# Kernel optimization log

Hardware: AMD Instinct MI355X
Metric: run time of the kernel (lower is better)

The kernel has to match this reference:

```python
import jax, jax.numpy as jnp
import numpy as np

B, S, H = 2, 2048, 2048
NH, NKV = 16, 4
HD = H // NH            # 128
GROUPS = NH // NKV      # 4
ROTARY_BASE = 10000.0
NEG = -1e9


def setup_inputs() -> dict:
    key = jax.random.key(0)
    ks = jax.random.split(key, 6)
    x = jax.random.normal(ks[0], (B, S, H), dtype=jnp.float32)
    # additive causal mask [B,1,S,S]
    causal = jnp.where(jnp.tril(jnp.ones((S, S), dtype=bool)), 0.0, NEG).astype(jnp.float32)
    attention_mask = jnp.broadcast_to(causal[None, None], (B, 1, S, S))
    position_ids = jnp.broadcast_to(jnp.arange(S, dtype=jnp.int32)[None], (B, S))
    sc = 0.02
    Wq = jax.random.normal(ks[1], (H, NH * HD), dtype=jnp.float32) * sc
    Wk = jax.random.normal(ks[2], (H, NKV * HD), dtype=jnp.float32) * sc
    Wv = jax.random.normal(ks[3], (H, NKV * HD), dtype=jnp.float32) * sc
    Wo = jax.random.normal(ks[4], (H, H), dtype=jnp.float32) * sc
    return {"x": x, "attention_mask": attention_mask, "position_ids": position_ids,
            "Wq": Wq, "Wk": Wk, "Wv": Wv, "Wo": Wo}


def _rotate_half(t):
    t1, t2 = t[..., : HD // 2], t[..., HD // 2:]
    return jnp.concatenate((-t2, t1), axis=-1)


def _rope_sin_cos(position_ids, dtype):
    inv_freq = 1.0 / (ROTARY_BASE ** (jnp.arange(0, HD, 2, dtype=jnp.float32) / HD))  # [HD/2]
    freqs = position_ids.astype(jnp.float32)[..., None] * inv_freq[None, None, :]      # [B,S,HD/2]
    emb = jnp.concatenate((freqs, freqs), axis=-1)                                     # [B,S,HD]
    return jnp.sin(emb).astype(dtype), jnp.cos(emb).astype(dtype)


def reference(x, attention_mask, position_ids, Wq, Wk, Wv, Wo):
    # QKV projections (no bias)
    q = (x @ Wq).reshape(B, S, NH, HD).transpose(0, 2, 1, 3)     # [B,NH,S,HD]
    k = (x @ Wk).reshape(B, S, NKV, HD).transpose(0, 2, 1, 3)    # [B,NKV,S,HD]
    v = (x @ Wv).reshape(B, S, NKV, HD).transpose(0, 2, 1, 3)
    sin, cos = _rope_sin_cos(position_ids, x.dtype)
    sin, cos = sin[:, None], cos[:, None]                         # unsqueeze head dim
    q = q * cos + _rotate_half(q) * sin
    k = k * cos + _rotate_half(k) * sin
    # GQA: repeat kv heads
    k = jnp.repeat(k, GROUPS, axis=1)                             # [B,NH,S,HD]
    v = jnp.repeat(v, GROUPS, axis=1)
    scores = jnp.einsum('bhqd,bhkd->bhqk', q, k) / jnp.sqrt(jnp.asarray(HD, x.dtype))
    scores = scores + attention_mask                              # additive causal mask
    attn = jax.nn.softmax(scores.astype(jnp.float32), axis=-1).astype(x.dtype)
    # dropout p=0.0 -> no-op
    out = jnp.einsum('bhqk,bhkd->bhqd', attn, v)                  # [B,NH,S,HD]
    out = out.transpose(0, 2, 1, 3).reshape(B, S, H)
    return out @ Wo
```

## Files before the change

kernel.cpp:

```cpp
#include <hip/hip_runtime.h>
#include <hip/hip_bf16.h>
#include <stdint.h>
#include <math.h>

#define B_ 2
#define S_ 2048
#define H_ 2048
#define NH_ 16
#define NKV_ 4
#define HD_ 128

typedef __bf16 bf16;
typedef __bf16 bf16x8 __attribute__((ext_vector_type(8)));
typedef __bf16 bf16x4 __attribute__((ext_vector_type(4)));
typedef float f32x4 __attribute__((ext_vector_type(4)));

__device__ __forceinline__ void async_copy16(const void* g, void* l) {
  __builtin_amdgcn_global_load_lds(
      (const __attribute__((address_space(1))) void*)(uintptr_t)g,
      (__attribute__((address_space(3))) void*)(uintptr_t)l,
      16, 0, 0);
}

__device__ __forceinline__ f32x4 mfma16(bf16x8 a, bf16x8 b, f32x4 c) {
  return __builtin_amdgcn_mfma_f32_16x16x32_bf16(a, b, c, 0, 0, 0);
}


__global__ void f32_to_bf16_k(const float* __restrict__ in, bf16* __restrict__ o, int n) {
  int i = (blockIdx.x * 256 + threadIdx.x) * 4;
  if (i >= n) return;
  float4 v = *(const float4*)(in + i);
  bf16x4 r;
  r[0] = (bf16)v.x; r[1] = (bf16)v.y; r[2] = (bf16)v.z; r[3] = (bf16)v.w;
  *(bf16x4*)(o + i) = r;
}

__global__ void transpose_to_bf16_k(const float* __restrict__ W, bf16* __restrict__ Wt,
                                    int K, int N) {
  __shared__ float tile[32][33];
  int n0 = blockIdx.x * 32, k0 = blockIdx.y * 32;
  int tx = threadIdx.x, ty = threadIdx.y;
#pragma unroll
  for (int j = 0; j < 32; j += 8)
    tile[ty + j][tx] = W[(size_t)(k0 + ty + j) * N + n0 + tx];
  __syncthreads();
#pragma unroll
  for (int j = 0; j < 32; j += 8)
    Wt[(size_t)(n0 + ty + j) * K + k0 + tx] = (bf16)tile[tx][ty + j];
}

__global__ void rope_table_k(float2* __restrict__ tab) {
  int i = blockIdx.x * 256 + threadIdx.x;
  int p = i >> 6, d = i & 63;
  float invf = expf(-((float)(2 * d) / 128.0f) * 9.210340371976184f);
  float fr = (float)p * invf;
  float sv, cv;
  sincosf(fr, &sv, &cv);
  tab[i] = make_float2(cv, sv);
}

__global__ void rope_apply_k(bf16* __restrict__ t, const int* __restrict__ pos_ids,
                             const float2* __restrict__ tab, int hshift, int hmask,
                             float scale) {
  int i = blockIdx.x * 256 + threadIdx.x;
  int d = i & 63;
  int tmp = i >> 6;
  int h = tmp & hmask;
  int row = tmp >> hshift;
  int pos = pos_ids[row];
  float2 cs = tab[pos * 64 + d];
  size_t base = (((size_t)row << hshift) + h) * HD_;
  float a = (float)t[base + d];
  float b = (float)t[base + d + 64];
  t[base + d]      = (bf16)((a * cs.x - b * cs.y) * scale);
  t[base + d + 64] = (bf16)((b * cs.x + a * cs.y) * scale);
}


template <bool OUT_F32>
__global__ __launch_bounds__(512) void gemm8_k(const bf16* __restrict__ A,
                                               const bf16* __restrict__ Bt,
                                               void* __restrict__ Cv,
                                               int M, int N, int K) {
  extern __shared__ __align__(16) char smem[];
  const int tid = threadIdx.x;
  const int lane = tid & 63;
  const int w = tid >> 6;
  const int wm = w >> 2;
  const int wn = w & 3;
  const int g16 = lane >> 4, c16 = lane & 15;
  const int row0 = blockIdx.y * 128;
  const int col0 = blockIdx.x * 256;
  const int srow = tid >> 3;
  const int sslot = tid & 7;
  const int ldsw = w * 1024;

  auto stageA = [&](int s, int kt, int r) {
    int row = r * 64 + srow;
    int ss = sslot ^ (row & 7);
    async_copy16(A + (size_t)(row0 + row) * K + (kt << 6) + ss * 8,
                 smem + s * 49152 + r * 8192 + ldsw);
  };
  auto stageB = [&](int s, int kt, int r) {
    int row = r * 64 + srow;
    int ss = sslot ^ (row & 7);
    async_copy16(Bt + (size_t)(col0 + row) * K + (kt << 6) + ss * 8,
                 smem + s * 49152 + 16384 + r * 8192 + ldsw);
  };

  int offA[2][4], offB[2][4];
#pragma unroll
  for (int ks = 0; ks < 2; ++ks) {
#pragma unroll
    for (int i = 0; i < 4; ++i) {
      int ra = wm * 64 + i * 16 + c16;
      offA[ks][i] = ra * 128 + (((ks * 4 + g16) ^ (ra & 7)) << 4);
      int rb = wn * 64 + i * 16 + c16;
      offB[ks][i] = rb * 128 + (((ks * 4 + g16) ^ (rb & 7)) << 4);
    }
  }

  const f32x4 fz = {0.f, 0.f, 0.f, 0.f};
  f32x4 acc[4][4];
#pragma unroll
  for (int i = 0; i < 4; ++i)
#pragma unroll
    for (int j = 0; j < 4; ++j) acc[i][j] = fz;

  const int nkt = K >> 6;
#pragma unroll
  for (int r = 0; r < 2; ++r) stageA(0, 0, r);
#pragma unroll
  for (int r = 0; r < 4; ++r) stageB(0, 0, r);
#pragma unroll
  for (int r = 0; r < 2; ++r) stageA(1, 1, r);
#pragma unroll
  for (int r = 0; r < 4; ++r) stageB(1, 1, r);
  asm volatile("s_waitcnt vmcnt(6)" ::: "memory");
  __builtin_amdgcn_s_barrier();

  int ct = 0, pt = 2;
  for (int t = 0; t < nkt; ++t) {
    const char* Ab = smem + ct * 49152;
    const char* Bb = Ab + 16384;
    const bool pf = (t + 2 < nkt);
    const int kpf = t + 2;
    bf16x8 a0[4], a1[4], bx[2];

#pragma unroll
    for (int i = 0; i < 4; ++i) a0[i] = *(const bf16x8*)(Ab + offA[0][i]);
    bx[0] = *(const bf16x8*)(Bb + offB[0][0]);
    bx[1] = *(const bf16x8*)(Bb + offB[0][1]);
    if (pf) { stageA(pt, kpf, 0); stageA(pt, kpf, 1); }
    asm volatile("" ::: "memory");
    __builtin_amdgcn_s_barrier();
    asm volatile("s_waitcnt lgkmcnt(0)" ::: "memory");
    __builtin_amdgcn_sched_barrier(0);
    __builtin_amdgcn_s_setprio(1);
#pragma unroll
    for (int i = 0; i < 4; ++i) {
      acc[i][0] = mfma16(a0[i], bx[0], acc[i][0]);
      acc[i][1] = mfma16(a0[i], bx[1], acc[i][1]);
    }
    __builtin_amdgcn_s_setprio(0);
    __builtin_amdgcn_sched_barrier(0);
    asm volatile("" ::: "memory");
    __builtin_amdgcn_s_barrier();

    bx[0] = *(const bf16x8*)(Bb + offB[0][2]);
    bx[1] = *(const bf16x8*)(Bb + offB[0][3]);
    if (pf) { stageB(pt, kpf, 0); stageB(pt, kpf, 1); }
    asm volatile("" ::: "memory");
    __builtin_amdgcn_s_barrier();
    asm volatile("s_waitcnt lgkmcnt(0)" ::: "memory");
    __builtin_amdgcn_sched_barrier(0);
    __builtin_amdgcn_s_setprio(1);
#pragma unroll
    for (int i = 0; i < 4; ++i) {
      acc[i][2] = mfma16(a0[i], bx[0], acc[i][2]);
      acc[i][3] = mfma16(a0[i], bx[1], acc[i][3]);
    }
    __builtin_amdgcn_s_setprio(0);
    __builtin_amdgcn_sched_barrier(0);
    asm volatile("" ::: "memory");
    __builtin_amdgcn_s_barrier();

#pragma unroll
    for (int i = 0; i < 4; ++i) a1[i] = *(const bf16x8*)(Ab + offA[1][i]);
    bx[0] = *(const bf16x8*)(Bb + offB[1][0]);
    bx[1] = *(const bf16x8*)(Bb + offB[1][1]);
    if (pf) { stageB(pt, kpf, 2); stageB(pt, kpf, 3); }
    asm volatile("" ::: "memory");
    __builtin_amdgcn_s_barrier();
    asm volatile("s_waitcnt lgkmcnt(0)" ::: "memory");
    __builtin_amdgcn_sched_barrier(0);
    __builtin_amdgcn_s_setprio(1);
#pragma unroll
    for (int i = 0; i < 4; ++i) {
      acc[i][0] = mfma16(a1[i], bx[0], acc[i][0]);
      acc[i][1] = mfma16(a1[i], bx[1], acc[i][1]);
    }
    __builtin_amdgcn_s_setprio(0);
    __builtin_amdgcn_sched_barrier(0);
    asm volatile("" ::: "memory");
    __builtin_amdgcn_s_barrier();

    bx[0] = *(const bf16x8*)(Bb + offB[1][2]);
    bx[1] = *(const bf16x8*)(Bb + offB[1][3]);
    if (pf) asm volatile("s_waitcnt vmcnt(6)" ::: "memory");
    else    asm volatile("s_waitcnt vmcnt(0)" ::: "memory");
    __builtin_amdgcn_s_barrier();
    asm volatile("s_waitcnt lgkmcnt(0)" ::: "memory");
    __builtin_amdgcn_sched_barrier(0);
    __builtin_amdgcn_s_setprio(1);
#pragma unroll
    for (int i = 0; i < 4; ++i) {
      acc[i][2] = mfma16(a1[i], bx[0], acc[i][2]);
      acc[i][3] = mfma16(a1[i], bx[1], acc[i][3]);
    }
    __builtin_amdgcn_s_setprio(0);
    __builtin_amdgcn_sched_barrier(0);
    asm volatile("" ::: "memory");
    __builtin_amdgcn_s_barrier();

    ct = (ct == 2) ? 0 : ct + 1;
    pt = (pt == 2) ? 0 : pt + 1;
  }

#pragma unroll
  for (int i = 0; i < 4; ++i) {
    int gr0 = row0 + wm * 64 + i * 16 + g16 * 4;
#pragma unroll
    for (int j = 0; j < 4; ++j) {
      int gc = col0 + wn * 64 + j * 16 + c16;
#pragma unroll
      for (int r = 0; r < 4; ++r) {
        if constexpr (OUT_F32)
          ((float*)Cv)[(size_t)(gr0 + r) * N + gc] = acc[i][j][r];
        else
          ((bf16*)Cv)[(size_t)(gr0 + r) * N + gc] = (bf16)acc[i][j][r];
      }
    }
  }
}


template <bool OUT_F32, bool VT_Z1>
__global__ __launch_bounds__(256) void gemm_bt_k(const bf16* __restrict__ A,
                                                 const bf16* __restrict__ Bt0,
                                                 const bf16* __restrict__ Bt1,
                                                 void* __restrict__ C0, void* __restrict__ C1,
                                                 int M, int N, int K) {
  const bf16* __restrict__ Bt = (blockIdx.z == 0) ? Bt0 : Bt1;
  void* C = (blockIdx.z == 0) ? C0 : C1;
  __shared__ __align__(16) bf16 As[128 * 64];
  __shared__ __align__(16) bf16 Bs[128 * 64];
  const int tid = threadIdx.x;
  const int lane = tid & 63;
  const int w = tid >> 6;
  const int wm = w >> 1, wn = w & 1;
  const int g16 = lane >> 4, c16 = lane & 15;
  const int row0 = blockIdx.y * 128;
  const int col0 = blockIdx.x * 128;
  const int sr = lane >> 3;
  const int st = lane & 7;
  const int ss = st ^ sr;

  const f32x4 fz = {0.f, 0.f, 0.f, 0.f};
  f32x4 acc[4][4];
#pragma unroll
  for (int i = 0; i < 4; ++i)
#pragma unroll
    for (int j = 0; j < 4; ++j) acc[i][j] = fz;

  const int nkt = K >> 6;
  for (int kt = 0; kt < nkt; ++kt) {
    const int k0 = kt << 6;
    __syncthreads();
#pragma unroll
    for (int c = 0; c < 4; ++c) {
      int rbase = w * 32 + c * 8;
      async_copy16(A + (size_t)(row0 + rbase + sr) * K + k0 + ss * 8,
                   (char*)As + rbase * 128);
      async_copy16(Bt + (size_t)(col0 + rbase + sr) * K + k0 + ss * 8,
                   (char*)Bs + rbase * 128);
    }
    __syncthreads();
#pragma unroll
    for (int ks = 0; ks < 2; ++ks) {
      bf16x8 af[4], bfr[4];
#pragma unroll
      for (int t = 0; t < 4; ++t) {
        int ra = wm * 64 + t * 16 + c16;
        af[t] = *(const bf16x8*)((const char*)As + ra * 128 + (((ks * 4 + g16) ^ (ra & 7)) << 4));
        int rb = wn * 64 + t * 16 + c16;
        bfr[t] = *(const bf16x8*)((const char*)Bs + rb * 128 + (((ks * 4 + g16) ^ (rb & 7)) << 4));
      }
#pragma unroll
      for (int i = 0; i < 4; ++i)
#pragma unroll
        for (int j = 0; j < 4; ++j) acc[i][j] = mfma16(af[i], bfr[j], acc[i][j]);
    }
  }

  const bool vt = VT_Z1 && (blockIdx.z == 1);
#pragma unroll
  for (int i = 0; i < 4; ++i) {
    int gr0 = row0 + wm * 64 + i * 16 + g16 * 4;
#pragma unroll
    for (int j = 0; j < 4; ++j) {
      int gc = col0 + wn * 64 + j * 16 + c16;
      if (vt) {
        size_t va = ((size_t)((gr0 >> 11) * NKV_ + (gc >> 7)) * HD_ + (gc & 127)) * S_ + (gr0 & 2047);
        bf16x4 pk;
#pragma unroll
        for (int r = 0; r < 4; ++r) pk[r] = (bf16)acc[i][j][r];
        *(bf16x4*)((bf16*)C + va) = pk;
      } else {
#pragma unroll
        for (int r = 0; r < 4; ++r) {
          if constexpr (OUT_F32)
            ((float*)C)[(size_t)(gr0 + r) * N + gc] = acc[i][j][r];
          else
            ((bf16*)C)[(size_t)(gr0 + r) * N + gc] = (bf16)acc[i][j][r];
        }
      }
    }
  }
}


__global__ __launch_bounds__(256, 2) void attn_fwd_k(const bf16* __restrict__ Qg,
                                                     const bf16* __restrict__ Kg,
                                                     const bf16* __restrict__ VTg,
                                                     bf16* __restrict__ Og) {
  __shared__ __align__(16) bf16 Ks[2][64 * 128];
  __shared__ __align__(16) bf16 Vt[2][128 * 64];

  const int tid = threadIdx.x;
  const int lane = tid & 63;
  const int w = tid >> 6;
  const int g16 = lane >> 4;
  const int c16 = lane & 15;

  int bid = blockIdx.x;
  int rr_ = bid >> 5, bh = bid & 31;
  int qb = (rr_ < 8) ? (15 - rr_) : (rr_ - 8);
  const int b = bh >> 4;
  const int h = bh & 15;
  const int hkv = h >> 2;
  const int q0 = qb * 128;
  const int qw = q0 + w * 32;

  bf16x8 qf[2][4];
#pragma unroll
  for (int nq = 0; nq < 2; ++nq)
#pragma unroll
    for (int ksq = 0; ksq < 4; ++ksq)
      qf[nq][ksq] = *(const bf16x8*)(Qg + ((size_t)(b * S_ + qw + nq * 16 + c16) * NH_ + h) * HD_ + (ksq * 4 + g16) * 8);

  float m_run[2] = {-1e30f, -1e30f};
  float l_run[2] = {0.f, 0.f};
  const f32x4 fz = {0.f, 0.f, 0.f, 0.f};
  f32x4 acc[2][8];
#pragma unroll
  for (int nq = 0; nq < 2; ++nq)
#pragma unroll
    for (int dt = 0; dt < 8; ++dt) acc[nq][dt] = fz;

  const size_t kbase = ((size_t)b * S_ * NKV_ + hkv) * HD_;
  const size_t vbase = ((size_t)(b * NKV_ + hkv)) * HD_ * S_;

  auto stage = [&](int buf, int kv0) {
#pragma unroll
    for (int rd = 0; rd < 4; ++rd) {
      int Lb = rd * 256 + w * 64;
      int row = (Lb + lane) >> 4;
      int ssl = (lane & 15) ^ (row & 7);
      async_copy16(Kg + kbase + (size_t)(kv0 + row) * (NKV_ * HD_) + ssl * 8,
                   (char*)&Ks[buf][0] + Lb * 16);
    }
#pragma unroll
    for (int rd = 0; rd < 4; ++rd) {
      int Lb = rd * 256 + w * 64;
      int row = (Lb + lane) >> 3;
      int ssl = (lane & 7) ^ (row & 7);
      async_copy16(VTg + vbase + (size_t)row * S_ + kv0 + ssl * 8,
                   (char*)&Vt[buf][0] + Lb * 16);
    }
  };

  const int ntiles = 2 * qb + 2;
  stage(0, 0);
  int cur = 0;

  for (int t = 0; t < ntiles; ++t) {
    __syncthreads();
    if (t + 1 < ntiles) stage(cur ^ 1, (t + 1) * 64);
    const int kv0 = t * 64;

    if (kv0 <= qw + 31) {
      const bf16* KsC = &Ks[cur][0];
      const bf16* VtC = &Vt[cur][0];

      f32x4 sc[2][4];
#pragma unroll
      for (int nq = 0; nq < 2; ++nq)
#pragma unroll
        for (int mt = 0; mt < 4; ++mt) sc[nq][mt] = fz;

#pragma unroll
      for (int ksq = 0; ksq < 4; ++ksq) {
        bf16x8 kf[4];
#pragma unroll
        for (int mt = 0; mt < 4; ++mt) {
          int gp = c16 >> 2, rp = c16 & 3;
          int blk = 8 * (mt >> 1) + 2 * gp + ((mt & 1) ^ (gp & 1));
          int row = blk * 4 + rp;
          kf[mt] = *(const bf16x8*)((const char*)KsC + row * 256 + (((ksq * 4 + g16) ^ (row & 7)) << 4));
        }
#pragma unroll
        for (int nq = 0; nq < 2; ++nq)
#pragma unroll
          for (int mt = 0; mt < 4; ++mt)
            sc[nq][mt] = mfma16(kf[mt], qf[nq][ksq], sc[nq][mt]);
      }

      if (kv0 + 63 > qw) {
#pragma unroll
        for (int nq = 0; nq < 2; ++nq) {
          int qa = qw + nq * 16 + c16;
#pragma unroll
          for (int mt = 0; mt < 4; ++mt) {
            int blk = 8 * (mt >> 1) + 2 * g16 + ((mt & 1) ^ (g16 & 1));
#pragma unroll
            for (int r = 0; r < 4; ++r) {
              int ka = kv0 + blk * 4 + r;
              if (ka > qa) sc[nq][mt][r] = -1e30f;
            }
          }
        }
      }

      float mx[2];
#pragma unroll
      for (int nq = 0; nq < 2; ++nq) {
        float v = sc[nq][0][0];
#pragma unroll
        for (int mt = 0; mt < 4; ++mt)
#pragma unroll
          for (int r = 0; r < 4; ++r) v = fmaxf(v, sc[nq][mt][r]);
        v = fmaxf(v, __shfl_xor(v, 16));
        v = fmaxf(v, __shfl_xor(v, 32));
        mx[nq] = v;
      }
      if (__any((mx[0] > m_run[0] + 8.f) || (mx[1] > m_run[1] + 8.f))) {
#pragma unroll
        for (int nq = 0; nq < 2; ++nq) {
          float mn = fmaxf(m_run[nq], mx[nq]);
          float corr = exp2f(m_run[nq] - mn);
          m_run[nq] = mn;
          l_run[nq] *= corr;
#pragma unroll
          for (int dt = 0; dt < 8; ++dt) acc[nq][dt] *= corr;
        }
      }
#pragma unroll
      for (int nq = 0; nq < 2; ++nq) {
        float sum = 0.f;
#pragma unroll
        for (int mt = 0; mt < 4; ++mt)
#pragma unroll
          for (int r = 0; r < 4; ++r) {
            float p = exp2f(sc[nq][mt][r] - m_run[nq]);
            sc[nq][mt][r] = p;
            sum += p;
          }
        sum += __shfl_xor(sum, 16);
        sum += __shfl_xor(sum, 32);
        l_run[nq] += sum;
      }

      bf16x8 pa[2][2];
#pragma unroll
      for (int nq = 0; nq < 2; ++nq)
#pragma unroll
        for (int ks = 0; ks < 2; ++ks) {
          f32x4 sA = (g16 & 1) ? sc[nq][2 * ks + 1] : sc[nq][2 * ks];
          f32x4 sB = (g16 & 1) ? sc[nq][2 * ks] : sc[nq][2 * ks + 1];
          bf16x8 tf;
          tf[0] = (bf16)sA[0]; tf[1] = (bf16)sA[1]; tf[2] = (bf16)sA[2]; tf[3] = (bf16)sA[3];
          tf[4] = (bf16)sB[0]; tf[5] = (bf16)sB[1]; tf[6] = (bf16)sB[2]; tf[7] = (bf16)sB[3];
          pa[nq][ks] = tf;
        }

#pragma unroll
      for (int ks = 0; ks < 2; ++ks)
#pragma unroll
        for (int dt = 0; dt < 8; ++dt) {
          int rv = dt * 16 + c16;
          bf16x8 vf = *(const bf16x8*)((const char*)VtC + rv * 128 + (((ks * 4 + g16) ^ (rv & 7)) << 4));
          acc[0][dt] = mfma16(vf, pa[0][ks], acc[0][dt]);
          acc[1][dt] = mfma16(vf, pa[1][ks], acc[1][dt]);
        }
    }
    cur ^= 1;
  }

#pragma unroll
  for (int nq = 0; nq < 2; ++nq) {
    float inv = 1.0f / l_run[nq];
    size_t base = ((size_t)(b * S_ + qw + nq * 16 + c16) * NH_ + h) * HD_ + g16 * 4;
#pragma unroll
    for (int dt = 0; dt < 8; ++dt) {
      bf16x4 ov;
#pragma unroll
      for (int r = 0; r < 4; ++r) ov[r] = (bf16)(acc[nq][dt][r] * inv);
      *(bf16x4*)(Og + base + dt * 16) = ov;
    }
  }
}


extern "C" void kernel_launch(void* const* d_in, const int* in_sizes, int n_in,
                              void* d_out, int out_size, void* d_ws, size_t ws_size,
                              hipStream_t stream) {
  const float* x  = (const float*)d_in[0];
  const int* pos  = (const int*)d_in[2];
  const float* Wq = (const float*)d_in[3];
  const float* Wk = (const float*)d_in[4];
  const float* Wv = (const float*)d_in[5];
  const float* Wo = (const float*)d_in[6];

  char* ws = (char*)d_ws;
  size_t off = 0;
  auto alloc = [&](size_t bytes) -> char* {
    char* p = ws + off;
    off += (bytes + 255) & ~(size_t)255;
    return p;
  };
  const size_t rows = (size_t)B_ * S_;
  bf16* xb   = (bf16*)alloc(rows * H_ * 2);
  bf16* bq   = (bf16*)alloc(rows * (NH_ * HD_) * 2);
  bf16* batt = (bf16*)alloc(rows * (NH_ * HD_) * 2);
  bf16* WqT  = (bf16*)alloc((size_t)H_ * (NH_ * HD_) * 2);
  bf16* WoT  = (bf16*)alloc((size_t)H_ * H_ * 2);
  bf16* bk   = (bf16*)alloc(rows * (NKV_ * HD_) * 2);
  bf16* VT   = (bf16*)alloc(rows * (NKV_ * HD_) * 2);
  bf16* WkT  = (bf16*)alloc((size_t)H_ * (NKV_ * HD_) * 2);
  bf16* WvT  = (bf16*)alloc((size_t)H_ * (NKV_ * HD_) * 2);
  float2* tab = (float2*)alloc((size_t)S_ * 64 * sizeof(float2));

  auto* fq = gemm8_k<false>;
  auto* fo = gemm8_k<true>;
  const int dynlds = 3 * 49152;
  bool big =
      (hipFuncSetAttribute((const void*)fq, hipFuncAttributeMaxDynamicSharedMemorySize, dynlds) == hipSuccess) &&
      (hipFuncSetAttribute((const void*)fo, hipFuncAttributeMaxDynamicSharedMemorySize, dynlds) == hipSuccess);

  f32_to_bf16_k<<<(rows * H_) / (256 * 4), 256, 0, stream>>>(x, xb, rows * H_);
  transpose_to_bf16_k<<<dim3(H_ / 32, H_ / 32), dim3(32, 8), 0, stream>>>(Wq, WqT, H_, NH_ * HD_);
  transpose_to_bf16_k<<<dim3((NKV_ * HD_) / 32, H_ / 32), dim3(32, 8), 0, stream>>>(Wk, WkT, H_, NKV_ * HD_);
  transpose_to_bf16_k<<<dim3((NKV_ * HD_) / 32, H_ / 32), dim3(32, 8), 0, stream>>>(Wv, WvT, H_, NKV_ * HD_);
  transpose_to_bf16_k<<<dim3(H_ / 32, H_ / 32), dim3(32, 8), 0, stream>>>(Wo, WoT, H_, H_);
  rope_table_k<<<(S_ * 64) / 256, 256, 0, stream>>>(tab);

  if (big)
    gemm8_k<false><<<dim3(8, 32), 512, dynlds, stream>>>(xb, WqT, bq, 4096, 2048, 2048);
  else
    gemm_bt_k<false, false><<<dim3(16, 32, 1), 256, 0, stream>>>(xb, WqT, WqT, bq, bq, 4096, 2048, 2048);

  gemm_bt_k<false, true><<<dim3(4, 32, 2), 256, 0, stream>>>(xb, WkT, WvT, bk, VT, 4096, 512, 2048);

  rope_apply_k<<<(4096 * NH_ * 64) / 256, 256, 0, stream>>>(bq, pos, tab, 4, 15, 0.12753102f);
  rope_apply_k<<<(4096 * NKV_ * 64) / 256, 256, 0, stream>>>(bk, pos, tab, 2, 3, 1.0f);

  attn_fwd_k<<<dim3(512), 256, 0, stream>>>(bq, bk, VT, batt);

  if (big)
    gemm8_k<true><<<dim3(8, 32), 512, dynlds, stream>>>(batt, WoT, d_out, 4096, 2048, 2048);
  else
    gemm_bt_k<true, false><<<dim3(16, 32, 1), 256, 0, stream>>>(batt, WoT, WoT, d_out, d_out, 4096, 2048, 2048);
}
```

Before: 226.9 us.

## Fuse QKV projections into one GEMM, widen attention warps, simplify GEMM pipeline

```diff
diff --git a/kernel.cpp b/kernel.cpp
--- a/kernel.cpp
+++ b/kernel.cpp
@@ -78,10 +78,12 @@
 }
 
 
-template <bool OUT_F32>
+template <int MODE>
 __global__ __launch_bounds__(512) void gemm8_k(const bf16* __restrict__ A,
                                                const bf16* __restrict__ Bt,
-                                               void* __restrict__ Cv,
+                                               void* __restrict__ C0,
+                                               void* __restrict__ C1,
+                                               void* __restrict__ C2,
                                                int M, int N, int K) {
   extern __shared__ __align__(16) char smem[];
   const int tid = threadIdx.x;
@@ -146,68 +148,30 @@
     const char* Bb = Ab + 16384;
     const bool pf = (t + 2 < nkt);
     const int kpf = t + 2;
-    bf16x8 a0[4], a1[4], bx[2];
-
-#pragma unroll
-    for (int i = 0; i < 4; ++i) a0[i] = *(const bf16x8*)(Ab + offA[0][i]);
-    bx[0] = *(const bf16x8*)(Bb + offB[0][0]);
-    bx[1] = *(const bf16x8*)(Bb + offB[0][1]);
-    if (pf) { stageA(pt, kpf, 0); stageA(pt, kpf, 1); }
-    asm volatile("" ::: "memory");
+    bf16x8 af[4], bfr[4];
+
+#pragma unroll
+    for (int i = 0; i < 4; ++i) af[i] = *(const bf16x8*)(Ab + offA[0][i]);
+#pragma unroll
+    for (int j = 0; j < 4; ++j) bfr[j] = *(const bf16x8*)(Bb + offB[0][j]);
+    if (pf) { stageA(pt, kpf, 0); stageA(pt, kpf, 1); stageB(pt, kpf, 0); }
     __builtin_amdgcn_s_barrier();
     asm volatile("s_waitcnt lgkmcnt(0)" ::: "memory");
     __builtin_amdgcn_sched_barrier(0);
     __builtin_amdgcn_s_setprio(1);
 #pragma unroll
-    for (int i = 0; i < 4; ++i) {
-      acc[i][0] = mfma16(a0[i], bx[0], acc[i][0]);
-      acc[i][1] = mfma16(a0[i], bx[1], acc[i][1]);
-    }
+    for (int i = 0; i < 4; ++i)
+#pragma unroll
+      for (int j = 0; j < 4; ++j) acc[i][j] = mfma16(af[i], bfr[j], acc[i][j]);
     __builtin_amdgcn_s_setprio(0);
     __builtin_amdgcn_sched_barrier(0);
-    asm volatile("" ::: "memory");
     __builtin_amdgcn_s_barrier();
 
-    bx[0] = *(const bf16x8*)(Bb + offB[0][2]);
-    bx[1] = *(const bf16x8*)(Bb + offB[0][3]);
-    if (pf) { stageB(pt, kpf, 0); stageB(pt, kpf, 1); }
-    asm volatile("" ::: "memory");
-    __builtin_amdgcn_s_barrier();
-    asm volatile("s_waitcnt lgkmcnt(0)" ::: "memory");
-    __builtin_amdgcn_sched_barrier(0);
-    __builtin_amdgcn_s_setprio(1);
-#pragma unroll
-    for (int i = 0; i < 4; ++i) {
-      acc[i][2] = mfma16(a0[i], bx[0], acc[i][2]);
-      acc[i][3] = mfma16(a0[i], bx[1], acc[i][3]);
-    }
-    __builtin_amdgcn_s_setprio(0);
-    __builtin_amdgcn_sched_barrier(0);
-    asm volatile("" ::: "memory");
-    __builtin_amdgcn_s_barrier();
-
-#pragma unroll
-    for (int i = 0; i < 4; ++i) a1[i] = *(const bf16x8*)(Ab + offA[1][i]);
-    bx[0] = *(const bf16x8*)(Bb + offB[1][0]);
-    bx[1] = *(const bf16x8*)(Bb + offB[1][1]);
-    if (pf) { stageB(pt, kpf, 2); stageB(pt, kpf, 3); }
-    asm volatile("" ::: "memory");
-    __builtin_amdgcn_s_barrier();
-    asm volatile("s_waitcnt lgkmcnt(0)" ::: "memory");
-    __builtin_amdgcn_sched_barrier(0);
-    __builtin_amdgcn_s_setprio(1);
-#pragma unroll
-    for (int i = 0; i < 4; ++i) {
-      acc[i][0] = mfma16(a1[i], bx[0], acc[i][0]);
-      acc[i][1] = mfma16(a1[i], bx[1], acc[i][1]);
-    }
-    __builtin_amdgcn_s_setprio(0);
-    __builtin_amdgcn_sched_barrier(0);
-    asm volatile("" ::: "memory");
-    __builtin_amdgcn_s_barrier();
-
-    bx[0] = *(const bf16x8*)(Bb + offB[1][2]);
-    bx[1] = *(const bf16x8*)(Bb + offB[1][3]);
+#pragma unroll
+    for (int i = 0; i < 4; ++i) af[i] = *(const bf16x8*)(Ab + offA[1][i]);
+#pragma unroll
+    for (int j = 0; j < 4; ++j) bfr[j] = *(const bf16x8*)(Bb + offB[1][j]);
+    if (pf) { stageB(pt, kpf, 1); stageB(pt, kpf, 2); stageB(pt, kpf, 3); }
     if (pf) asm volatile("s_waitcnt vmcnt(6)" ::: "memory");
     else    asm volatile("s_waitcnt vmcnt(0)" ::: "memory");
     __builtin_amdgcn_s_barrier();
@@ -215,13 +179,11 @@
     __builtin_amdgcn_sched_barrier(0);
     __builtin_amdgcn_s_setprio(1);
 #pragma unroll
-    for (int i = 0; i < 4; ++i) {
-      acc[i][2] = mfma16(a1[i], bx[0], acc[i][2]);
-      acc[i][3] = mfma16(a1[i], bx[1], acc[i][3]);
-    }
+    for (int i = 0; i < 4; ++i)
+#pragma unroll
+      for (int j = 0; j < 4; ++j) acc[i][j] = mfma16(af[i], bfr[j], acc[i][j]);
     __builtin_amdgcn_s_setprio(0);
     __builtin_amdgcn_sched_barrier(0);
-    asm volatile("" ::: "memory");
     __builtin_amdgcn_s_barrier();
 
     ct = (ct == 2) ? 0 : ct + 1;
@@ -234,12 +196,32 @@
 #pragma unroll
     for (int j = 0; j < 4; ++j) {
       int gc = col0 + wn * 64 + j * 16 + c16;
-#pragma unroll
-      for (int r = 0; r < 4; ++r) {
-        if constexpr (OUT_F32)
-          ((float*)Cv)[(size_t)(gr0 + r) * N + gc] = acc[i][j][r];
-        else
-          ((bf16*)Cv)[(size_t)(gr0 + r) * N + gc] = (bf16)acc[i][j][r];
+      if constexpr (MODE == 2) {
+        if (col0 < 2048) {
+#pragma unroll
+          for (int r = 0; r < 4; ++r)
+            ((bf16*)C0)[(size_t)(gr0 + r) * 2048 + gc] = (bf16)acc[i][j][r];
+        } else if (col0 < 2560) {
+#pragma unroll
+          for (int r = 0; r < 4; ++r)
+            ((bf16*)C1)[(size_t)(gr0 + r) * 512 + (gc - 2048)] = (bf16)acc[i][j][r];
+        } else {
+          int dv = gc - 2560;
+          int hkv = dv >> 7, d = dv & 127;
+          size_t va = (((size_t)(gr0 >> 11) * NKV_ + hkv) * HD_ + d) * S_ + (gr0 & 2047);
+          bf16x4 pk;
+#pragma unroll
+          for (int r = 0; r < 4; ++r) pk[r] = (bf16)acc[i][j][r];
+          *(bf16x4*)((bf16*)C2 + va) = pk;
+        }
+      } else {
+#pragma unroll
+        for (int r = 0; r < 4; ++r) {
+          if constexpr (MODE == 1)
+            ((float*)C0)[(size_t)(gr0 + r) * N + gc] = acc[i][j][r];
+          else
+            ((bf16*)C0)[(size_t)(gr0 + r) * N + gc] = (bf16)acc[i][j][r];
+        }
       }
     }
   }
@@ -331,7 +313,7 @@
 }
 
 
-__global__ __launch_bounds__(256, 2) void attn_fwd_k(const bf16* __restrict__ Qg,
+__global__ __launch_bounds__(128, 1) void attn_fwd_k(const bf16* __restrict__ Qg,
                                                      const bf16* __restrict__ Kg,
                                                      const bf16* __restrict__ VTg,
                                                      bf16* __restrict__ Og) {
@@ -351,21 +333,40 @@
   const int h = bh & 15;
   const int hkv = h >> 2;
   const int q0 = qb * 128;
-  const int qw = q0 + w * 32;
-
-  bf16x8 qf[2][4];
-#pragma unroll
-  for (int nq = 0; nq < 2; ++nq)
+  const int qw = q0 + w * 64;
+
+  bf16x8 qf[4][4];
+#pragma unroll
+  for (int nq = 0; nq < 4; ++nq)
 #pragma unroll
     for (int ksq = 0; ksq < 4; ++ksq)
       qf[nq][ksq] = *(const bf16x8*)(Qg + ((size_t)(b * S_ + qw + nq * 16 + c16) * NH_ + h) * HD_ + (ksq * 4 + g16) * 8);
 
-  float m_run[2] = {-1e30f, -1e30f};
-  float l_run[2] = {0.f, 0.f};
+  int kfo[4][4];
+#pragma unroll
+  for (int ksq = 0; ksq < 4; ++ksq)
+#pragma unroll
+    for (int mt = 0; mt < 4; ++mt) {
+      int gp = c16 >> 2, rp = c16 & 3;
+      int blk = 8 * (mt >> 1) + 2 * gp + ((mt & 1) ^ (gp & 1));
+      int row = blk * 4 + rp;
+      kfo[ksq][mt] = row * 256 + (((ksq * 4 + g16) ^ (row & 7)) << 4);
+    }
+  int vfo[2][8];
+#pragma unroll
+  for (int ks = 0; ks < 2; ++ks)
+#pragma unroll
+    for (int dt = 0; dt < 8; ++dt) {
+      int rv = dt * 16 + c16;
+      vfo[ks][dt] = rv * 128 + (((ks * 4 + g16) ^ (rv & 7)) << 4);
+    }
+
+  float m_run[4] = {-1e30f, -1e30f, -1e30f, -1e30f};
+  float l_run[4] = {0.f, 0.f, 0.f, 0.f};
   const f32x4 fz = {0.f, 0.f, 0.f, 0.f};
-  f32x4 acc[2][8];
-#pragma unroll
-  for (int nq = 0; nq < 2; ++nq)
+  f32x4 acc[4][8];
+#pragma unroll
+  for (int nq = 0; nq < 4; ++nq)
 #pragma unroll
     for (int dt = 0; dt < 8; ++dt) acc[nq][dt] = fz;
 
@@ -374,20 +375,20 @@
 
   auto stage = [&](int buf, int kv0) {
 #pragma unroll
-    for (int rd = 0; rd < 4; ++rd) {
-      int Lb = rd * 256 + w * 64;
-      int row = (Lb + lane) >> 4;
-      int ssl = (lane & 15) ^ (row & 7);
+    for (int rd = 0; rd < 8; ++rd) {
+      int idx = rd * 128 + tid;
+      int row = idx >> 4;
+      int ssl = (idx & 15) ^ (row & 7);
       async_copy16(Kg + kbase + (size_t)(kv0 + row) * (NKV_ * HD_) + ssl * 8,
-                   (char*)&Ks[buf][0] + Lb * 16);
-    }
-#pragma unroll
-    for (int rd = 0; rd < 4; ++rd) {
-      int Lb = rd * 256 + w * 64;
-      int row = (Lb + lane) >> 3;
-      int ssl = (lane & 7) ^ (row & 7);
+                   (char*)&Ks[buf][0] + (rd * 128 + w * 64) * 16);
+    }
+#pragma unroll
+    for (int rd = 0; rd < 8; ++rd) {
+      int idx = rd * 128 + tid;
+      int row = idx >> 3;
+      int ssl = (idx & 7) ^ (row & 7);
       async_copy16(VTg + vbase + (size_t)row * S_ + kv0 + ssl * 8,
-                   (char*)&Vt[buf][0] + Lb * 16);
+                   (char*)&Vt[buf][0] + (rd * 128 + w * 64) * 16);
     }
   };
 
@@ -400,13 +401,13 @@
     if (t + 1 < ntiles) stage(cur ^ 1, (t + 1) * 64);
     const int kv0 = t * 64;
 
-    if (kv0 <= qw + 31) {
-      const bf16* KsC = &Ks[cur][0];
-      const bf16* VtC = &Vt[cur][0];
-
-      f32x4 sc[2][4];
-#pragma unroll
-      for (int nq = 0; nq < 2; ++nq)
+    if (kv0 <= qw + 63) {
+      const char* KsC = (const char*)&Ks[cur][0];
+      const char* VtC = (const char*)&Vt[cur][0];
+
+      f32x4 sc[4][4];
+#pragma unroll
+      for (int nq = 0; nq < 4; ++nq)
 #pragma unroll
         for (int mt = 0; mt < 4; ++mt) sc[nq][mt] = fz;
 
@@ -414,14 +415,10 @@
       for (int ksq = 0; ksq < 4; ++ksq) {
         bf16x8 kf[4];
 #pragma unroll
-        for (int mt = 0; mt < 4; ++mt) {
-          int gp = c16 >> 2, rp = c16 & 3;
-          int blk = 8 * (mt >> 1) + 2 * gp + ((mt & 1) ^ (gp & 1));
-          int row = blk * 4 + rp;
-          kf[mt] = *(const bf16x8*)((const char*)KsC + row * 256 + (((ksq * 4 + g16) ^ (row & 7)) << 4));
-        }
-#pragma unroll
-        for (int nq = 0; nq < 2; ++nq)
+        for (int mt = 0; mt < 4; ++mt)
+          kf[mt] = *(const bf16x8*)(KsC + kfo[ksq][mt]);
+#pragma unroll
+        for (int nq = 0; nq < 4; ++nq)
 #pragma unroll
           for (int mt = 0; mt < 4; ++mt)
             sc[nq][mt] = mfma16(kf[mt], qf[nq][ksq], sc[nq][mt]);
@@ -429,7 +426,7 @@
 
       if (kv0 + 63 > qw) {
 #pragma unroll
-        for (int nq = 0; nq < 2; ++nq) {
+        for (int nq = 0; nq < 4; ++nq) {
           int qa = qw + nq * 16 + c16;
 #pragma unroll
           for (int mt = 0; mt < 4; ++mt) {
@@ -443,9 +440,9 @@
         }
       }
 
-      float mx[2];
-#pragma unroll
-      for (int nq = 0; nq < 2; ++nq) {
+      float mx[4];
+#pragma unroll
+      for (int nq = 0; nq < 4; ++nq) {
         float v = sc[nq][0][0];
 #pragma unroll
         for (int mt = 0; mt < 4; ++mt)
@@ -455,9 +452,11 @@
         v = fmaxf(v, __shfl_xor(v, 32));
         mx[nq] = v;
       }
-      if (__any((mx[0] > m_run[0] + 8.f) || (mx[1] > m_run[1] + 8.f))) {
-#pragma unroll
-        for (int nq = 0; nq < 2; ++nq) {
+      bool need = (mx[0] > m_run[0] + 8.f) || (mx[1] > m_run[1] + 8.f) ||
+                  (mx[2] > m_run[2] + 8.f) || (mx[3] > m_run[3] + 8.f);
+      if (__any(need)) {
+#pragma unroll
+        for (int nq = 0; nq < 4; ++nq) {
           float mn = fmaxf(m_run[nq], mx[nq]);
           float corr = exp2f(m_run[nq] - mn);
           m_run[nq] = mn;
@@ -467,7 +466,7 @@
         }
       }
 #pragma unroll
-      for (int nq = 0; nq < 2; ++nq) {
+      for (int nq = 0; nq < 4; ++nq) {
         float sum = 0.f;
 #pragma unroll
         for (int mt = 0; mt < 4; ++mt)
@@ -482,9 +481,9 @@
         l_run[nq] += sum;
       }
 
-      bf16x8 pa[2][2];
-#pragma unroll
-      for (int nq = 0; nq < 2; ++nq)
+      bf16x8 pa[4][2];
+#pragma unroll
+      for (int nq = 0; nq < 4; ++nq)
 #pragma unroll
         for (int ks = 0; ks < 2; ++ks) {
           f32x4 sA = (g16 & 1) ? sc[nq][2 * ks + 1] : sc[nq][2 * ks];
@@ -499,17 +498,17 @@
       for (int ks = 0; ks < 2; ++ks)
 #pragma unroll
         for (int dt = 0; dt < 8; ++dt) {
-          int rv = dt * 16 + c16;
-          bf16x8 vf = *(const bf16x8*)((const char*)VtC + rv * 128 + (((ks * 4 + g16) ^ (rv & 7)) << 4));
-          acc[0][dt] = mfma16(vf, pa[0][ks], acc[0][dt]);
-          acc[1][dt] = mfma16(vf, pa[1][ks], acc[1][dt]);
+          bf16x8 vf = *(const bf16x8*)(VtC + vfo[ks][dt]);
+#pragma unroll
+          for (int nq = 0; nq < 4; ++nq)
+            acc[nq][dt] = mfma16(vf, pa[nq][ks], acc[nq][dt]);
         }
     }
     cur ^= 1;
   }
 
 #pragma unroll
-  for (int nq = 0; nq < 2; ++nq) {
+  for (int nq = 0; nq < 4; ++nq) {
     float inv = 1.0f / l_run[nq];
     size_t base = ((size_t)(b * S_ + qw + nq * 16 + c16) * NH_ + h) * HD_ + g16 * 4;
 #pragma unroll
@@ -541,22 +540,24 @@
     return p;
   };
   const size_t rows = (size_t)B_ * S_;
-  bf16* xb   = (bf16*)alloc(rows * H_ * 2);
-  bf16* bq   = (bf16*)alloc(rows * (NH_ * HD_) * 2);
-  bf16* batt = (bf16*)alloc(rows * (NH_ * HD_) * 2);
-  bf16* WqT  = (bf16*)alloc((size_t)H_ * (NH_ * HD_) * 2);
-  bf16* WoT  = (bf16*)alloc((size_t)H_ * H_ * 2);
-  bf16* bk   = (bf16*)alloc(rows * (NKV_ * HD_) * 2);
-  bf16* VT   = (bf16*)alloc(rows * (NKV_ * HD_) * 2);
-  bf16* WkT  = (bf16*)alloc((size_t)H_ * (NKV_ * HD_) * 2);
-  bf16* WvT  = (bf16*)alloc((size_t)H_ * (NKV_ * HD_) * 2);
+  bf16* xb    = (bf16*)alloc(rows * H_ * 2);
+  bf16* bq    = (bf16*)alloc(rows * (NH_ * HD_) * 2);
+  bf16* batt  = (bf16*)alloc(rows * (NH_ * HD_) * 2);
+  bf16* WqkvT = (bf16*)alloc((size_t)3072 * H_ * 2);
+  bf16* WoT   = (bf16*)alloc((size_t)H_ * H_ * 2);
+  bf16* bk    = (bf16*)alloc(rows * (NKV_ * HD_) * 2);
+  bf16* VT    = (bf16*)alloc(rows * (NKV_ * HD_) * 2);
   float2* tab = (float2*)alloc((size_t)S_ * 64 * sizeof(float2));
 
-  auto* fq = gemm8_k<false>;
-  auto* fo = gemm8_k<true>;
+  bf16* WqT = WqkvT;
+  bf16* WkT = WqkvT + (size_t)2048 * H_;
+  bf16* WvT = WqkvT + (size_t)2560 * H_;
+
+  auto* fqkv = gemm8_k<2>;
+  auto* fo   = gemm8_k<1>;
   const int dynlds = 3 * 49152;
   bool big =
-      (hipFuncSetAttribute((const void*)fq, hipFuncAttributeMaxDynamicSharedMemorySize, dynlds) == hipSuccess) &&
+      (hipFuncSetAttribute((const void*)fqkv, hipFuncAttributeMaxDynamicSharedMemorySize, dynlds) == hipSuccess) &&
       (hipFuncSetAttribute((const void*)fo, hipFuncAttributeMaxDynamicSharedMemorySize, dynlds) == hipSuccess);
 
   f32_to_bf16_k<<<(rows * H_) / (256 * 4), 256, 0, stream>>>(x, xb, rows * H_);
@@ -566,20 +567,20 @@
   transpose_to_bf16_k<<<dim3(H_ / 32, H_ / 32), dim3(32, 8), 0, stream>>>(Wo, WoT, H_, H_);
   rope_table_k<<<(S_ * 64) / 256, 256, 0, stream>>>(tab);
 
-  if (big)
-    gemm8_k<false><<<dim3(8, 32), 512, dynlds, stream>>>(xb, WqT, bq, 4096, 2048, 2048);
-  else
+  if (big) {
+    gemm8_k<2><<<dim3(12, 32), 512, dynlds, stream>>>(xb, WqkvT, bq, bk, VT, 4096, 3072, 2048);
+  } else {
     gemm_bt_k<false, false><<<dim3(16, 32, 1), 256, 0, stream>>>(xb, WqT, WqT, bq, bq, 4096, 2048, 2048);
-
-  gemm_bt_k<false, true><<<dim3(4, 32, 2), 256, 0, stream>>>(xb, WkT, WvT, bk, VT, 4096, 512, 2048);
+    gemm_bt_k<false, true><<<dim3(4, 32, 2), 256, 0, stream>>>(xb, WkT, WvT, bk, VT, 4096, 512, 2048);
+  }
 
   rope_apply_k<<<(4096 * NH_ * 64) / 256, 256, 0, stream>>>(bq, pos, tab, 4, 15, 0.12753102f);
   rope_apply_k<<<(4096 * NKV_ * 64) / 256, 256, 0, stream>>>(bk, pos, tab, 2, 3, 1.0f);
 
-  attn_fwd_k<<<dim3(512), 256, 0, stream>>>(bq, bk, VT, batt);
+  attn_fwd_k<<<dim3(512), 128, 0, stream>>>(bq, bk, VT, batt);
 
   if (big)
-    gemm8_k<true><<<dim3(8, 32), 512, dynlds, stream>>>(batt, WoT, d_out, 4096, 2048, 2048);
+    gemm8_k<1><<<dim3(8, 32), 512, dynlds, stream>>>(batt, WoT, d_out, nullptr, nullptr, 4096, 2048, 2048);
   else
     gemm_bt_k<true, false><<<dim3(16, 32, 1), 256, 0, stream>>>(batt, WoT, WoT, d_out, d_out, 4096, 2048, 2048);
 }
```

Result: slower. 310.0 us (+36.6%).
